# Optimization experiments

Hardware: AMD Instinct MI355X
Metric: run time of the kernel (lower is better)

Reference implementation:

```python
import jax, jax.numpy as jnp
import numpy as np
import math

B, T, C = 4, 2048, 1024
N_HEAD = 16
HEAD_DIM = C // N_HEAD


def setup_inputs() -> dict:
    key = jax.random.key(0)
    k1, k2, k3, k4, k5 = jax.random.split(key, 5)
    s = 1.0 / math.sqrt(C)
    return {
        "x": jax.random.normal(k1, (B, T, C), dtype=jnp.float32),
        "W_attn": jax.random.normal(k2, (3 * C, C), dtype=jnp.float32) * s,
        "b_attn": jax.random.normal(k3, (3 * C,), dtype=jnp.float32) * 0.02,
        "W_proj": jax.random.normal(k4, (C, C), dtype=jnp.float32) * s,
        "b_proj": jax.random.normal(k5, (C,), dtype=jnp.float32) * 0.02,
    }


def reference(x, W_attn, b_attn, W_proj, b_proj):
    Bx, Tx, Cx = x.shape
    # QKV projection (torch Linear: x @ W.T + b), split into q,k,v
    qkv = jnp.einsum("btc,dc->btd", x, W_attn) + b_attn  # [B,T,3C]
    q, k, v = jnp.split(qkv, 3, axis=-1)
    # [B,T,C] -> [B,H,T,hd]
    def to_heads(t):
        return t.reshape(Bx, Tx, N_HEAD, HEAD_DIM).transpose(0, 2, 1, 3)
    q, k, v = to_heads(q), to_heads(k), to_heads(v)
    scale = 1.0 / math.sqrt(HEAD_DIM)
    att = jnp.einsum("bhqd,bhkd->bhqk", q, k) * scale  # [B,H,T,T]
    causal = jnp.tril(jnp.ones((Tx, Tx), dtype=bool))
    att = jnp.where(causal, att, -jnp.inf)
    att = jax.nn.softmax(att, axis=-1)
    y = jnp.einsum("bhqk,bhkd->bhqd", att, v)  # [B,H,T,hd]
    y = y.transpose(0, 2, 1, 3).reshape(Bx, Tx, Cx)
    y = jnp.einsum("btc,dc->btd", y, W_proj) + b_proj
    return y
```

## Files before the change

### kernel.cpp

```cpp
#include <hip/hip_runtime.h>
#include <hip/hip_bf16.h>
#include <stdint.h>

typedef unsigned short u16;
typedef __attribute__((ext_vector_type(8))) short bf16x8;
typedef __attribute__((ext_vector_type(4))) short s16x4;
typedef __attribute__((ext_vector_type(4))) float f32x4;

#define B_SZ 4
#define T_SZ 2048
#define C_SZ 1024
#define NH   16
#define HD   64
#define LOG2E 1.44269504088896340736f

__device__ __forceinline__ u16 f2bf(float f) {
  unsigned int u = __float_as_uint(f);
  u += 0x7fffu + ((u >> 16) & 1u);
  return (u16)(u >> 16);
}
__device__ __forceinline__ u16 f2bf_hu(float f) {
  return (u16)((__float_as_uint(f) + 0x8000u) >> 16);
}
__device__ __forceinline__ void gload_lds16(const u16* g, u16* l) {
  __builtin_amdgcn_global_load_lds((const __attribute__((address_space(1))) void*)g,
                                   (__attribute__((address_space(3))) void*)l, 16, 0, 0);
}

__global__ void cast3_f32_bf16(const float* __restrict__ x, const float* __restrict__ wa,
                               const float* __restrict__ wp, u16* __restrict__ xb,
                               u16* __restrict__ wab, u16* __restrict__ wpb) {
  const int n1 = 8192 * 1024 / 8, n2 = 3072 * 1024 / 8, n3 = 1024 * 1024 / 8;
  int i = blockIdx.x * blockDim.x + threadIdx.x;
  const float* in; u16* out; int idx;
  if (i < n1)            { in = x;  out = xb;  idx = i; }
  else if (i < n1 + n2)  { in = wa; out = wab; idx = i - n1; }
  else if (i < n1 + n2 + n3) { in = wp; out = wpb; idx = i - n1 - n2; }
  else return;
  const float4* p = (const float4*)in + (size_t)idx * 2;
  float4 a = p[0], b = p[1];
  bf16x8 o;
  o[0] = (short)f2bf(a.x); o[1] = (short)f2bf(a.y);
  o[2] = (short)f2bf(a.z); o[3] = (short)f2bf(a.w);
  o[4] = (short)f2bf(b.x); o[5] = (short)f2bf(b.y);
  o[6] = (short)f2bf(b.z); o[7] = (short)f2bf(b.w);
  ((bf16x8*)out)[idx] = o;
}

#define GEMM128_PROLOG(A_, B_)                                                \
  extern __shared__ u16 lds[];                                                \
  u16* As = lds;                                         \
  u16* Bs = lds + 16384;                                 \
  const int tid = threadIdx.x;                                                \
  const int lane = tid & 63, w = tid >> 6;                                    \
  const int wm = w >> 1, wn = w & 1;                                          \
  const int quad = lane >> 4, l16 = lane & 15;                                \
  const int gx = gridDim.x;                                                   \
  const int nwg = gx * gridDim.y;                                             \
  const int wg0 = blockIdx.y * gx + blockIdx.x;                               \
  const int swz = (wg0 & 7) * (nwg >> 3) + (wg0 >> 3);                        \
  const int n0 = (swz % gx) * 128;                                            \
  const int m0 = (swz / gx) * 128;                                            \
  const int dr8 = lane >> 3;                                                  \
  const int dc8 = (lane & 7) ^ dr8;                                           \
  const u16* gAL = A_ + (size_t)(m0 + w * 32 + dr8) * K + dc8 * 8;            \
  const u16* gBL = B_ + (size_t)(n0 + w * 32 + dr8) * K + dc8 * 8;            \
  const int NT = K >> 6;                                                      \
  auto stageA = [&](int tile) {                                               \
    u16* d = As + (tile & 1) * 8192 + w * 2048;                               \
    const u16* g = gAL + (size_t)tile * 64;                                   \
    _Pragma("unroll")                                                         \
    for (int sg = 0; sg < 4; ++sg)                                            \
      gload_lds16(g + (size_t)(sg * 8) * K, d + sg * 512);                    \
  };                                                                          \
  auto stageB = [&](int tile) {                                               \
    u16* d = Bs + (tile & 1) * 8192 + w * 2048;                               \
    const u16* g = gBL + (size_t)tile * 64;                                   \
    _Pragma("unroll")                                                         \
    for (int sg = 0; sg < 4; ++sg)                                            \
      gload_lds16(g + (size_t)(sg * 8) * K, d + sg * 512);                    \
  };                                                                          \
  f32x4 acc[4][4];                                                            \
  _Pragma("unroll")                                                           \
  for (int i = 0; i < 4; i++)                                                 \
    _Pragma("unroll")                                                         \
    for (int j = 0; j < 4; j++) acc[i][j] = (f32x4){0.f, 0.f, 0.f, 0.f};      \
  stageA(0); stageB(0);                                                       \
  asm volatile("s_waitcnt vmcnt(0)" ::: "memory");                            \
  __builtin_amdgcn_s_barrier();                                               \
  const int sK0 = ((quad) ^ (l16 & 7)) * 8;                                   \
  const int sK1 = ((4 + quad) ^ (l16 & 7)) * 8;                               \
  for (int tile = 0; tile < NT; ++tile) {                                     \
    const u16* Ab = As + (tile & 1) * 8192;                                   \
    const u16* Bb = Bs + (tile & 1) * 8192;                                   \
    _Pragma("unroll")                                                         \
    for (int mp = 0; mp < 2; ++mp) {                                          \
      bf16x8 af[2][2], bfr[4][2];                                             \
      _Pragma("unroll")                                                       \
      for (int a = 0; a < 2; ++a) {                                           \
        const int ro = (wm * 64 + (mp * 2 + a) * 16 + l16) * 64;              \
        af[a][0] = *(const bf16x8*)&Ab[ro + sK0];                             \
        af[a][1] = *(const bf16x8*)&Ab[ro + sK1];                             \
      }                                                                       \
      _Pragma("unroll")                                                       \
      for (int nt = 0; nt < 4; ++nt) {                                        \
        const int ro = (wn * 64 + nt * 16 + l16) * 64;                        \
        bfr[nt][0] = *(const bf16x8*)&Bb[ro + sK0];                           \
        bfr[nt][1] = *(const bf16x8*)&Bb[ro + sK1];                           \
      }                                                                       \
      if (mp == 0 && tile + 1 < NT) { stageA(tile + 1); stageB(tile + 1); }   \
      asm volatile("s_waitcnt lgkmcnt(8)");                                   \
      asm volatile("" ::: "memory");                                          \
      __builtin_amdgcn_s_barrier();                                           \
      asm volatile("s_waitcnt lgkmcnt(0)" ::: "memory");                      \
      __builtin_amdgcn_sched_barrier(0);                                      \
      __builtin_amdgcn_s_setprio(1);                                          \
      _Pragma("unroll")                                                       \
      for (int a = 0; a < 2; ++a)                                             \
        _Pragma("unroll")                                                     \
        for (int nt = 0; nt < 4; ++nt) {                                      \
          f32x4 c = acc[mp * 2 + a][nt];                                      \
          c = __builtin_amdgcn_mfma_f32_16x16x32_bf16(af[a][0], bfr[nt][0], c, 0, 0, 0); \
          c = __builtin_amdgcn_mfma_f32_16x16x32_bf16(af[a][1], bfr[nt][1], c, 0, 0, 0); \
          acc[mp * 2 + a][nt] = c;                                            \
        }                                                                     \
      __builtin_amdgcn_s_setprio(0);                                          \
      if (mp == 1) asm volatile("s_waitcnt vmcnt(0)" ::: "memory");           \
      asm volatile("" ::: "memory");                                          \
      __builtin_amdgcn_s_barrier();                                           \
    }                                                                         \
  }

__launch_bounds__(256, 2)
__global__ void gemm128_qkv(const u16* __restrict__ A, const u16* __restrict__ Bw,
                            const float* __restrict__ bias,
                            u16* __restrict__ O0, u16* __restrict__ O1, u16* __restrict__ O2,
                            int M, int N, int K) {
  GEMM128_PROLOG(A, Bw)

  const int ncol = n0 + wn * 64;
  float bv[4];
#pragma unroll
  for (int nt = 0; nt < 4; nt++) bv[nt] = bias[ncol + nt * 16 + l16];

  const int nsec = ncol >> 10;
  const int hh = (ncol >> 6) & 15;
  if (nsec < 2) {
    u16* dst = (nsec == 0 ? O0 : O1);
    const float qs = (nsec == 0) ? (0.125f * LOG2E) : 1.0f;
#pragma unroll
    for (int mt = 0; mt < 4; mt++) {
      const int row = m0 + wm * 64 + mt * 16 + quad * 4;
      const int bb = row >> 11;
      const int t = row & 2047;
#pragma unroll
      for (int nt = 0; nt < 4; nt++) {
        const int dh = nt * 16 + l16;
        const size_t a = (((size_t)bb * NH + hh) * T_SZ + t) * HD + dh;
#pragma unroll
        for (int r = 0; r < 4; r++)
          dst[a + (size_t)r * HD] = f2bf((acc[mt][nt][r] + bv[nt]) * qs);
      }
    }
  } else {
    u16* vth = O2;
    u16* S = lds + (size_t)w * (64 * 88);
#pragma unroll
    for (int mt = 0; mt < 4; ++mt)
#pragma unroll
      for (int nt = 0; nt < 4; ++nt) {
        s16x4 pk;
#pragma unroll
        for (int r = 0; r < 4; ++r) pk[r] = (short)f2bf(acc[mt][nt][r] + bv[nt]);
        *(s16x4*)&S[(nt * 16 + l16) * 88 + mt * 16 + quad * 4] = pk;
      }
    const int tbase = m0 + wm * 64;
    const int bb = tbase >> 11;
    const int tb = tbase & 2047;
    const size_t vrow = ((size_t)bb * NH + hh) * HD;
    const int tc = (lane & 7) * 8;
#pragma unroll
    for (int i = 0; i < 8; ++i) {
      const int nr = i * 8 + (lane >> 3);
      bf16x8 vv = *(const bf16x8*)&S[nr * 88 + tc];
      *(bf16x8*)&vth[(vrow + nr) * T_SZ + tb + tc] = vv;
    }
  }
}

__launch_bounds__(256, 2)
__global__ void gemm128_proj(const u16* __restrict__ A, const u16* __restrict__ Bw,
                             const float* __restrict__ bias, float* __restrict__ Cout,
                             int M, int N, int K) {
  GEMM128_PROLOG(A, Bw)

  float bv[4];
#pragma unroll
  for (int nt = 0; nt < 4; nt++) bv[nt] = bias[n0 + wn * 64 + nt * 16 + l16];
#pragma unroll
  for (int mt = 0; mt < 4; mt++) {
    const int row = m0 + wm * 64 + mt * 16 + quad * 4;
#pragma unroll
    for (int nt = 0; nt < 4; nt++) {
      const int col = n0 + wn * 64 + nt * 16 + l16;
#pragma unroll
      for (int r = 0; r < 4; r++)
        Cout[(size_t)(row + r) * N + col] = acc[mt][nt][r] + bv[nt];
    }
  }
}

__device__ __forceinline__ void attn_step(
    int kb, int kbn, int w, int quad, int l16, int qt128, int sw0, int sw1,
    const u16* gK0, const u16* gK1, const u16* gV0, const u16* gV1,
    u16* KsF, u16* VsF, u16* PsW,
    const bf16x8 (&qf)[2][2], f32x4 (&o)[2][4], float (&l_i)[2][4]) {
  __syncthreads();

  if (kb + 1 < kbn) {
    const int nb = (kb + 1) & 1;
    const size_t ko = (size_t)(kb + 1) * 64 * HD;
    const int vo = (kb + 1) * 64;
    gload_lds16(gK0 + ko, KsF + nb * 4096 + (2 * w) * 512);
    gload_lds16(gK1 + ko, KsF + nb * 4096 + (2 * w + 1) * 512);
    gload_lds16(gV0 + vo, VsF + nb * 4096 + (2 * w) * 512);
    gload_lds16(gV1 + vo, VsF + nb * 4096 + (2 * w + 1) * 512);
  }

  if (kb == kbn - 1 && w < 2) return;

  const u16* Kb = KsF + (kb & 1) * 4096;
  const u16* Vb = VsF + (kb & 1) * 4096;
  const int kt0 = kb * 64;

  f32x4 s[2][4];
  __builtin_amdgcn_s_setprio(1);
#pragma unroll
  for (int nt = 0; nt < 4; nt++) {
    bf16x8 kf0 = *(const bf16x8*)&Kb[(nt * 16 + l16) * 64 + sw0];
    bf16x8 kf1 = *(const bf16x8*)&Kb[(nt * 16 + l16) * 64 + sw1];
#pragma unroll
    for (int m = 0; m < 2; m++) {
      f32x4 t0 = (f32x4){0.f, 0.f, 0.f, 0.f};
      t0 = __builtin_amdgcn_mfma_f32_16x16x32_bf16(qf[m][0], kf0, t0, 0, 0, 0);
      t0 = __builtin_amdgcn_mfma_f32_16x16x32_bf16(qf[m][1], kf1, t0, 0, 0, 0);
      s[m][nt] = t0;
    }
  }
  __builtin_amdgcn_s_setprio(0);

  bf16x8 p0a, p1a, p0b, p1b;
#pragma unroll
  for (int m = 0; m < 2; m++) {
    const int mrow = qt128 + w * 32 + m * 16;
    const int qr = mrow + quad * 4;
    const bool diag = (kt0 + 64 > mrow);

    if (diag) {
#pragma unroll
      for (int nt = 0; nt < 4; nt++) {
        const int dk = kt0 + nt * 16 + l16 - qr;
#pragma unroll
        for (int r = 0; r < 4; r++) {
          float v = (dk > r) ? -10000.f : s[m][nt][r];
          s[m][nt][r] = exp2f(v);
        }
      }
    } else {
#pragma unroll
      for (int nt = 0; nt < 4; nt++)
#pragma unroll
        for (int r = 0; r < 4; r++)
          s[m][nt][r] = exp2f(s[m][nt][r]);
    }
#pragma unroll
    for (int r = 0; r < 4; r++)
      l_i[m][r] += (s[m][0][r] + s[m][1][r]) + (s[m][2][r] + s[m][3][r]);

#pragma unroll
    for (int nt = 0; nt < 4; nt++)
#pragma unroll
      for (int r = 0; r < 4; r++)
        PsW[(quad * 4 + r) * 72 + nt * 16 + l16] = f2bf_hu(s[m][nt][r]);
    if (m == 0) {
      p0a = *(const bf16x8*)&PsW[l16 * 72 + quad * 8];
      p1a = *(const bf16x8*)&PsW[l16 * 72 + 32 + quad * 8];
    } else {
      p0b = *(const bf16x8*)&PsW[l16 * 72 + quad * 8];
      p1b = *(const bf16x8*)&PsW[l16 * 72 + 32 + quad * 8];
    }
  }

  __builtin_amdgcn_s_setprio(1);
#pragma unroll
  for (int nt = 0; nt < 4; nt++) {
    bf16x8 v0 = *(const bf16x8*)&Vb[(nt * 16 + l16) * 64 + sw0];
    bf16x8 v1 = *(const bf16x8*)&Vb[(nt * 16 + l16) * 64 + sw1];
    o[0][nt] = __builtin_amdgcn_mfma_f32_16x16x32_bf16(p0a, v0, o[0][nt], 0, 0, 0);
    o[0][nt] = __builtin_amdgcn_mfma_f32_16x16x32_bf16(p1a, v1, o[0][nt], 0, 0, 0);
    o[1][nt] = __builtin_amdgcn_mfma_f32_16x16x32_bf16(p0b, v0, o[1][nt], 0, 0, 0);
    o[1][nt] = __builtin_amdgcn_mfma_f32_16x16x32_bf16(p1b, v1, o[1][nt], 0, 0, 0);
  }
  __builtin_amdgcn_s_setprio(0);
}

__launch_bounds__(256, 3)
__global__ void attn_fused(const u16* __restrict__ qh, const u16* __restrict__ kh,
                           const u16* __restrict__ vth, u16* __restrict__ out) {
  __shared__ __align__(16) u16 Ks[2][64 * 64];
  __shared__ __align__(16) u16 Vs[2][64 * 64];
  __shared__ __align__(16) u16 Ps[4][16 * 72];
  const int qt = 15 - blockIdx.z;
  const int h = blockIdx.x, b = blockIdx.y;
  const int tid = threadIdx.x;
  const int lane = tid & 63, w = tid >> 6;
  const int quad = lane >> 4, l16 = lane & 15;
  const size_t bh = (size_t)b * NH + h;
  const u16* Kbase = kh + bh * T_SZ * HD;
  const u16* Vbase = vth + bh * HD * T_SZ;
  const int qt128 = qt * 128;

  const int dr = lane >> 3;
  const int dc = (lane & 7) ^ dr;
  const u16* gK0 = Kbase + (size_t)(2 * w * 8 + dr) * HD + dc * 8;
  const u16* gK1 = Kbase + (size_t)((2 * w + 1) * 8 + dr) * HD + dc * 8;
  const u16* gV0 = Vbase + (size_t)(2 * w * 8 + dr) * T_SZ + dc * 8;
  const u16* gV1 = Vbase + (size_t)((2 * w + 1) * 8 + dr) * T_SZ + dc * 8;
  u16* KsF = &Ks[0][0];
  u16* VsF = &Vs[0][0];
  u16* PsW = &Ps[w][0];

  bf16x8 qf[2][2];
#pragma unroll
  for (int m = 0; m < 2; m++) {
    const int t = qt128 + w * 32 + m * 16 + l16;
    const u16* qrow = qh + (bh * T_SZ + t) * HD;
    qf[m][0] = *(const bf16x8*)(qrow + quad * 8);
    qf[m][1] = *(const bf16x8*)(qrow + 32 + quad * 8);
  }

  f32x4 o[2][4];
  float l_i[2][4];
#pragma unroll
  for (int m = 0; m < 2; m++)
#pragma unroll
    for (int i = 0; i < 4; i++) {
      o[m][i] = (f32x4){0.f, 0.f, 0.f, 0.f};
      l_i[m][i] = 0.f;
    }

  const int kbn = 2 * qt + 2;
  const int sw0 = (quad ^ (l16 & 7)) * 8;
  const int sw1 = ((4 + quad) ^ (l16 & 7)) * 8;

  gload_lds16(gK0, KsF + (2 * w) * 512);
  gload_lds16(gK1, KsF + (2 * w + 1) * 512);
  gload_lds16(gV0, VsF + (2 * w) * 512);
  gload_lds16(gV1, VsF + (2 * w + 1) * 512);

  for (int kb = 0; kb < kbn; kb++)
    attn_step(kb, kbn, w, quad, l16, qt128, sw0, sw1,
              gK0, gK1, gV0, gV1, KsF, VsF, PsW, qf, o, l_i);

#pragma unroll
  for (int m = 0; m < 2; m++)
#pragma unroll
    for (int r = 0; r < 4; r++) {
      float v = l_i[m][r];
      v += __shfl_xor(v, 1);
      v += __shfl_xor(v, 2);
      v += __shfl_xor(v, 4);
      v += __shfl_xor(v, 8);
      const float inv = 1.f / v;
      const int t = qt128 + w * 32 + m * 16 + quad * 4 + r;
      const size_t orow = ((size_t)b * T_SZ + t) * C_SZ + (size_t)h * HD;
#pragma unroll
      for (int nt = 0; nt < 4; nt++)
        out[orow + nt * 16 + l16] = f2bf(o[m][nt][r] * inv);
    }
}

extern "C" void kernel_launch(void* const* d_in, const int* in_sizes, int n_in,
                              void* d_out, int out_size, void* d_ws, size_t ws_size,
                              hipStream_t stream) {
  (void)in_sizes; (void)n_in; (void)out_size; (void)ws_size;
  const float* x      = (const float*)d_in[0];
  const float* W_attn = (const float*)d_in[1];
  const float* b_attn = (const float*)d_in[2];
  const float* W_proj = (const float*)d_in[3];
  const float* b_proj = (const float*)d_in[4];
  float* out = (float*)d_out;

  char* ws = (char*)d_ws;
  u16* xb  = (u16*)ws;  ws += (size_t)8192 * 1024 * 2;
  u16* Wab = (u16*)ws;  ws += (size_t)3072 * 1024 * 2;
  u16* Wpb = (u16*)ws;  ws += (size_t)1024 * 1024 * 2;
  u16* qhb = (u16*)ws;  ws += (size_t)8192 * 1024 * 2;
  u16* khb = (u16*)ws;  ws += (size_t)8192 * 1024 * 2;
  u16* vtb = (u16*)ws;  ws += (size_t)8192 * 1024 * 2;
  u16* aob = (u16*)ws;

  dim3 blk(256);
  cast3_f32_bf16<<<6144, blk, 0, stream>>>(x, W_attn, W_proj, xb, Wab, Wpb);

  gemm128_qkv<<<dim3(3072 / 128, 8192 / 128), blk, 65536, stream>>>(
      xb, Wab, b_attn, qhb, khb, vtb, 8192, 3072, 1024);
  attn_fused<<<dim3(NH, B_SZ, 16), blk, 0, stream>>>(qhb, khb, vtb, aob);
  gemm128_proj<<<dim3(1024 / 128, 8192 / 128), blk, 65536, stream>>>(
      aob, Wpb, b_proj, out, 8192, 1024, 1024);
}
```

Measured before the change: 245.6 us.

## Pair causal query tiles in one 512-thread block sharing K/V loads

```diff
diff --git a/kernel.cpp b/kernel.cpp
--- a/kernel.cpp
+++ b/kernel.cpp
@@ -211,23 +211,21 @@
 }
 
 __device__ __forceinline__ void attn_step(
-    int kb, int kbn, int w, int quad, int l16, int qt128, int sw0, int sw1,
-    const u16* gK0, const u16* gK1, const u16* gV0, const u16* gV1,
+    int kb, int kbn_own, int kbn_hi, int w, int wl, int quad, int l16,
+    int qt128, int sw0, int sw1,
+    const u16* gK, const u16* gV,
     u16* KsF, u16* VsF, u16* PsW,
     const bf16x8 (&qf)[2][2], f32x4 (&o)[2][4], float (&l_i)[2][4]) {
   __syncthreads();
 
-  if (kb + 1 < kbn) {
+  if (kb + 1 < kbn_hi) {
     const int nb = (kb + 1) & 1;
-    const size_t ko = (size_t)(kb + 1) * 64 * HD;
-    const int vo = (kb + 1) * 64;
-    gload_lds16(gK0 + ko, KsF + nb * 4096 + (2 * w) * 512);
-    gload_lds16(gK1 + ko, KsF + nb * 4096 + (2 * w + 1) * 512);
-    gload_lds16(gV0 + vo, VsF + nb * 4096 + (2 * w) * 512);
-    gload_lds16(gV1 + vo, VsF + nb * 4096 + (2 * w + 1) * 512);
-  }
-
-  if (kb == kbn - 1 && w < 2) return;
+    gload_lds16(gK + (size_t)(kb + 1) * 64 * HD, KsF + nb * 4096 + w * 512);
+    gload_lds16(gV + (kb + 1) * 64,              VsF + nb * 4096 + w * 512);
+  }
+
+  if (kb >= kbn_own) return;
+  if (kb == kbn_own - 1 && wl < 2) return;
 
   const u16* Kb = KsF + (kb & 1) * 4096;
   const u16* Vb = VsF + (kb & 1) * 4096;
@@ -252,7 +250,7 @@
   bf16x8 p0a, p1a, p0b, p1b;
 #pragma unroll
   for (int m = 0; m < 2; m++) {
-    const int mrow = qt128 + w * 32 + m * 16;
+    const int mrow = qt128 + wl * 32 + m * 16;
     const int qr = mrow + quad * 4;
     const bool diag = (kt0 + 64 > mrow);
 
@@ -304,28 +302,29 @@
   __builtin_amdgcn_s_setprio(0);
 }
 
-__launch_bounds__(256, 3)
+__launch_bounds__(512, 4)
 __global__ void attn_fused(const u16* __restrict__ qh, const u16* __restrict__ kh,
                            const u16* __restrict__ vth, u16* __restrict__ out) {
   __shared__ __align__(16) u16 Ks[2][64 * 64];
   __shared__ __align__(16) u16 Vs[2][64 * 64];
-  __shared__ __align__(16) u16 Ps[4][16 * 72];
-  const int qt = 15 - blockIdx.z;
+  __shared__ __align__(16) u16 Ps[8][16 * 72];
+  const int qp = blockIdx.z;
+  const int qlo = qp, qhi = 15 - qp;
   const int h = blockIdx.x, b = blockIdx.y;
   const int tid = threadIdx.x;
   const int lane = tid & 63, w = tid >> 6;
+  const int wl = w & 3;
   const int quad = lane >> 4, l16 = lane & 15;
   const size_t bh = (size_t)b * NH + h;
   const u16* Kbase = kh + bh * T_SZ * HD;
   const u16* Vbase = vth + bh * HD * T_SZ;
-  const int qt128 = qt * 128;
+  const int qt_own = (w < 4) ? qhi : qlo;
+  const int qt128 = qt_own * 128;
 
   const int dr = lane >> 3;
   const int dc = (lane & 7) ^ dr;
-  const u16* gK0 = Kbase + (size_t)(2 * w * 8 + dr) * HD + dc * 8;
-  const u16* gK1 = Kbase + (size_t)((2 * w + 1) * 8 + dr) * HD + dc * 8;
-  const u16* gV0 = Vbase + (size_t)(2 * w * 8 + dr) * T_SZ + dc * 8;
-  const u16* gV1 = Vbase + (size_t)((2 * w + 1) * 8 + dr) * T_SZ + dc * 8;
+  const u16* gK = Kbase + (size_t)(w * 8 + dr) * HD + dc * 8;
+  const u16* gV = Vbase + (size_t)(w * 8 + dr) * T_SZ + dc * 8;
   u16* KsF = &Ks[0][0];
   u16* VsF = &Vs[0][0];
   u16* PsW = &Ps[w][0];
@@ -333,7 +332,7 @@
   bf16x8 qf[2][2];
 #pragma unroll
   for (int m = 0; m < 2; m++) {
-    const int t = qt128 + w * 32 + m * 16 + l16;
+    const int t = qt128 + wl * 32 + m * 16 + l16;
     const u16* qrow = qh + (bh * T_SZ + t) * HD;
     qf[m][0] = *(const bf16x8*)(qrow + quad * 8);
     qf[m][1] = *(const bf16x8*)(qrow + 32 + quad * 8);
@@ -349,18 +348,17 @@
       l_i[m][i] = 0.f;
     }
 
-  const int kbn = 2 * qt + 2;
+  const int kbn_own = 2 * qt_own + 2;
+  const int kbn_hi = 2 * qhi + 2;
   const int sw0 = (quad ^ (l16 & 7)) * 8;
   const int sw1 = ((4 + quad) ^ (l16 & 7)) * 8;
 
-  gload_lds16(gK0, KsF + (2 * w) * 512);
-  gload_lds16(gK1, KsF + (2 * w + 1) * 512);
-  gload_lds16(gV0, VsF + (2 * w) * 512);
-  gload_lds16(gV1, VsF + (2 * w + 1) * 512);
-
-  for (int kb = 0; kb < kbn; kb++)
-    attn_step(kb, kbn, w, quad, l16, qt128, sw0, sw1,
-              gK0, gK1, gV0, gV1, KsF, VsF, PsW, qf, o, l_i);
+  gload_lds16(gK, KsF + w * 512);
+  gload_lds16(gV, VsF + w * 512);
+
+  for (int kb = 0; kb < kbn_hi; kb++)
+    attn_step(kb, kbn_own, kbn_hi, w, wl, quad, l16, qt128, sw0, sw1,
+              gK, gV, KsF, VsF, PsW, qf, o, l_i);
 
 #pragma unroll
   for (int m = 0; m < 2; m++)
@@ -372,7 +370,7 @@
       v += __shfl_xor(v, 4);
       v += __shfl_xor(v, 8);
       const float inv = 1.f / v;
-      const int t = qt128 + w * 32 + m * 16 + quad * 4 + r;
+      const int t = qt128 + wl * 32 + m * 16 + quad * 4 + r;
       const size_t orow = ((size_t)b * T_SZ + t) * C_SZ + (size_t)h * HD;
 #pragma unroll
       for (int nt = 0; nt < 4; nt++)
@@ -405,7 +403,7 @@
 
   gemm128_qkv<<<dim3(3072 / 128, 8192 / 128), blk, 65536, stream>>>(
       xb, Wab, b_attn, qhb, khb, vtb, 8192, 3072, 1024);
-  attn_fused<<<dim3(NH, B_SZ, 16), blk, 0, stream>>>(qhb, khb, vtb, aob);
+  attn_fused<<<dim3(NH, B_SZ, 8), dim3(512), 0, stream>>>(qhb, khb, vtb, aob);
   gemm128_proj<<<dim3(1024 / 128, 8192 / 128), blk, 65536, stream>>>(
       aob, Wpb, b_proj, out, 8192, 1024, 1024);
 }
```

Measured after the change: 251.2 us. 1.02x slower.
